# Kernel tuning notes

Hardware: AMD Instinct MI355X
Metric: run time of the kernel (lower is better)

The kernel has to match this reference:

```python
import jax, jax.numpy as jnp
import numpy as np

D_MODEL = 1024
N_HEADS = 16
HEAD_DIM = D_MODEL // N_HEADS


def setup_inputs() -> dict:
    key = jax.random.key(0)
    k1, k2, k3 = jax.random.split(key, 3)
    scale = 1.0 / np.sqrt(D_MODEL)
    x = jax.random.normal(k1, (4, 2048, D_MODEL), dtype=jnp.float32)
    w_qkv = jax.random.normal(k2, (D_MODEL, 3 * D_MODEL), dtype=jnp.float32) * scale
    b_qkv = jnp.zeros((3 * D_MODEL,), dtype=jnp.float32)
    w_proj = jax.random.normal(k3, (D_MODEL, D_MODEL), dtype=jnp.float32) * scale
    b_proj = jnp.zeros((D_MODEL,), dtype=jnp.float32)
    return {"x": x, "w_qkv": w_qkv, "b_qkv": b_qkv, "w_proj": w_proj, "b_proj": b_proj}


def reference(x, w_qkv, b_qkv, w_proj, b_proj):
    B, T, C = x.shape
    H, Dh = N_HEADS, HEAD_DIM
    qkv = x @ w_qkv + b_qkv                       # (B, T, 3C)
    qkv = qkv.reshape(B, T, 3, H, Dh)
    q = qkv[:, :, 0].transpose(0, 2, 1, 3)        # (B, H, T, Dh)
    k = qkv[:, :, 1].transpose(0, 2, 1, 3)
    v = qkv[:, :, 2].transpose(0, 2, 1, 3)
    att = jnp.einsum('bhqd,bhkd->bhqk', q, k) / jnp.sqrt(jnp.float32(Dh))
    causal = jnp.tril(jnp.ones((T, T), dtype=bool))
    att = jnp.where(causal[None, None], att, -jnp.inf)
    att = jax.nn.softmax(att, axis=-1)
    y = jnp.einsum('bhqk,bhkd->bhqd', att, v)     # (B, H, T, Dh)
    y = y.transpose(0, 2, 1, 3).reshape(B, T, C)
    return y @ w_proj + b_proj
```

## Files before the change

### kernel.cpp

```cpp
#include <hip/hip_runtime.h>
#include <hip/hip_bf16.h>
#include <math.h>

typedef __bf16 bf16_t;
typedef __bf16 bf16x4 __attribute__((ext_vector_type(4)));
typedef __bf16 bf16x8 __attribute__((ext_vector_type(8)));
typedef float floatx4 __attribute__((ext_vector_type(4)));

#define AS1 __attribute__((address_space(1)))
#define AS3 __attribute__((address_space(3)))

__device__ bf16_t g_xb[8192 * 1024];
__device__ bf16_t g_wqkvT[3072 * 1024];
__device__ bf16_t g_wprojT[1024 * 1024];
__device__ float  g_bqkv[3072];
__device__ float  g_bproj[1024];
__device__ bf16_t g_qkv[3ull * 64 * 2048 * 64];
#define HBREG (64ull * 2048 * 64)

__global__ __launch_bounds__(256) void cvt_x(const float* __restrict__ src, int n) {
  int i0 = (blockIdx.x * 256 + threadIdx.x) * 8;
  if (i0 >= n) return;
  const float4* s = (const float4*)src;
  float4 a = s[i0 / 4], b = s[i0 / 4 + 1];
  bf16x8 v;
  v[0] = (bf16_t)a.x; v[1] = (bf16_t)a.y; v[2] = (bf16_t)a.z; v[3] = (bf16_t)a.w;
  v[4] = (bf16_t)b.x; v[5] = (bf16_t)b.y; v[6] = (bf16_t)b.z; v[7] = (bf16_t)b.w;
  *(bf16x8*)&g_xb[i0] = v;
}

__global__ __launch_bounds__(256) void cvt_bias(const float* __restrict__ src,
                                                int which, int n) {
  int i = blockIdx.x * 256 + threadIdx.x;
  if (i >= n) return;
  (which ? g_bproj : g_bqkv)[i] = src[i];
}

__global__ __launch_bounds__(256) void tr64(const float* __restrict__ in,
                                            int which, int R, int C) {
  __shared__ bf16_t tile[64][65];
  bf16_t* out = which ? g_wprojT : g_wqkvT;
  int r0 = blockIdx.y * 64, c0 = blockIdx.x * 64;
  int tid = threadIdx.x;
#pragma unroll
  for (int it = 0; it < 16; ++it) {
    int idx = tid + it * 256;
    int r = idx >> 6, c = idx & 63;
    tile[r][c] = (bf16_t)in[(size_t)(r0 + r) * C + (c0 + c)];
  }
  __syncthreads();
#pragma unroll
  for (int it = 0; it < 16; ++it) {
    int idx = tid + it * 256;
    int r = idx >> 6, c = idx & 63;
    out[(size_t)(c0 + r) * R + (r0 + c)] = tile[c][r];
  }
}

__global__ __launch_bounds__(256) void gemm_bt(float* __restrict__ out_ext,
                                               int M, int N, int K,
                                               int amode, int bsel, int cmode) {
  __shared__ bf16_t As[128 * 32];
  __shared__ bf16_t Bs[128 * 32];
  const bf16_t* A = (amode == 0) ? g_xb : g_qkv;
  const bf16_t* Bt = bsel ? g_wprojT : g_wqkvT;
  const float* bias = bsel ? g_bproj : g_bqkv;
  const int tid = threadIdx.x;
  const int m0 = blockIdx.y * 128, n0 = blockIdx.x * 128;
  const int lane = tid & 63, wave = tid >> 6;
  const int wm = wave >> 1, wn = wave & 1;
  const int quad = lane >> 4, l16 = lane & 15;
  const int wub = tid & ~63;

  floatx4 acc[4][4] = {};

  for (int k0 = 0; k0 < K; k0 += 32) {
#pragma unroll
    for (int it = 0; it < 2; ++it) {
      int idx = tid + it * 256;
      int row = idx >> 2;
      int c8 = (idx & 3) * 8;
      int wbase = (it * 256 + wub) * 8;
      const bf16_t* asrc;
      if (amode == 0) {
        asrc = &A[(size_t)(m0 + row) * K + k0 + c8];
      } else {
        int m = m0 + row;
        int b = m >> 11, t = m & 2047;
        int h = k0 >> 6, dd = (k0 & 63) + c8;
        asrc = &A[((size_t)((b * 16 + h) * 2048 + t)) * 64 + dd];
      }
      const bf16_t* bsrc = &Bt[(size_t)(n0 + row) * K + k0 + c8];
      __builtin_amdgcn_global_load_lds((const AS1 void*)asrc,
                                       (AS3 void*)&As[wbase], 16, 0, 0);
      __builtin_amdgcn_global_load_lds((const AS1 void*)bsrc,
                                       (AS3 void*)&Bs[wbase], 16, 0, 0);
    }
    __syncthreads();
    bf16x8 af[4], bfr[4];
#pragma unroll
    for (int t = 0; t < 4; ++t) {
      af[t] = *(const bf16x8*)&As[(wm * 64 + t * 16 + l16) * 32 + quad * 8];
      bfr[t] = *(const bf16x8*)&Bs[(wn * 64 + t * 16 + l16) * 32 + quad * 8];
    }
#pragma unroll
    for (int tm = 0; tm < 4; ++tm)
#pragma unroll
      for (int tn = 0; tn < 4; ++tn)
        acc[tm][tn] = __builtin_amdgcn_mfma_f32_16x16x32_bf16(
            af[tm], bfr[tn], acc[tm][tn], 0, 0, 0);
    __syncthreads();
  }

#pragma unroll
  for (int tm = 0; tm < 4; ++tm) {
#pragma unroll
    for (int tn = 0; tn < 4; ++tn) {
      int ncol = n0 + wn * 64 + tn * 16 + l16;
      float bb = bias[ncol];
      int mbase = m0 + wm * 64 + tm * 16 + quad * 4;
      if (cmode == 0) {
        int which = ncol >> 10;
        int h = (ncol >> 6) & 15;
        int d = ncol & 63;
        int b = mbase >> 11, t = mbase & 2047;
        if (which == 2) {
          bf16x4 pk;
#pragma unroll
          for (int r = 0; r < 4; ++r) pk[r] = (bf16_t)(acc[tm][tn][r] + bb);
          size_t dst = 2 * HBREG + ((size_t)((b * 16 + h) * 64 + d)) * 2048 + t;
          *(bf16x4*)&g_qkv[dst] = pk;
        } else {
          size_t base = (size_t)which * HBREG +
                        ((size_t)((b * 16 + h) * 2048 + t)) * 64 + d;
#pragma unroll
          for (int r = 0; r < 4; ++r)
            g_qkv[base + (size_t)r * 64] = (bf16_t)(acc[tm][tn][r] + bb);
        }
      } else {
#pragma unroll
        for (int r = 0; r < 4; ++r)
          out_ext[(size_t)(mbase + r) * N + ncol] = acc[tm][tn][r] + bb;
      }
    }
  }
}

__global__ __launch_bounds__(256) void attn64() {
  const int LDW = 72;
  __shared__ bf16_t Qs[64 * 72];
  __shared__ bf16_t Ks[64 * 72];
  __shared__ bf16_t Vt[64 * 72];
  __shared__ bf16_t Ps[64 * 72];
  const float C1 = 0.1803368801111204f;
  const float C2 = -23.083120654223414f;
  const int tid = threadIdx.x;
  const int qpair = blockIdx.x;
  const int bh = blockIdx.y;
  const bf16_t* Qb  = g_qkv + (size_t)bh * 2048 * 64;
  const bf16_t* Kb  = g_qkv + HBREG + (size_t)bh * 2048 * 64;
  const bf16_t* VTb = g_qkv + 2 * HBREG + (size_t)bh * 64 * 2048;
  bf16_t* Yb = g_qkv + (size_t)bh * 2048 * 64;
  const int lane = tid & 63, wave = tid >> 6;
  const int quad = lane >> 4, l16 = lane & 15;
  const int row0 = tid >> 3, c80 = (tid & 7) * 8;

  bf16x8 ones8;
#pragma unroll
  for (int j = 0; j < 8; ++j) ones8[j] = (bf16_t)1.0f;

  for (int ph = 0; ph < 2; ++ph) {
    const int qi = ph ? (31 - qpair) : qpair;
    const int q0 = qi * 64;

    *(bf16x8*)&Qs[row0 * LDW + c80] =
        *(const bf16x8*)&Qb[(size_t)(q0 + row0) * 64 + c80];
    *(bf16x8*)&Qs[(row0 + 32) * LDW + c80] =
        *(const bf16x8*)&Qb[(size_t)(q0 + row0 + 32) * 64 + c80];
    __syncthreads();
    bf16x8 aq0 = *(const bf16x8*)&Qs[(wave * 16 + l16) * LDW + quad * 8];
    bf16x8 aq1 = *(const bf16x8*)&Qs[(wave * 16 + l16) * LDW + 32 + quad * 8];

    floatx4 o[4] = {};
    floatx4 osum = {};

    bf16x8 kp0 = *(const bf16x8*)&Kb[(size_t)row0 * 64 + c80];
    bf16x8 kp1 = *(const bf16x8*)&Kb[(size_t)(row0 + 32) * 64 + c80];
    bf16x8 vp0 = *(const bf16x8*)&VTb[(size_t)row0 * 2048 + c80];
    bf16x8 vp1 = *(const bf16x8*)&VTb[(size_t)(row0 + 32) * 2048 + c80];

    const int ntiles = qi + 1;
    for (int kt = 0; kt < ntiles; ++kt) {
      __syncthreads();
      *(bf16x8*)&Ks[row0 * LDW + c80] = kp0;
      *(bf16x8*)&Ks[(row0 + 32) * LDW + c80] = kp1;
      *(bf16x8*)&Vt[row0 * LDW + c80] = vp0;
      *(bf16x8*)&Vt[(row0 + 32) * LDW + c80] = vp1;
      if (kt + 1 < ntiles) {
        const int k1 = (kt + 1) * 64;
        kp0 = *(const bf16x8*)&Kb[(size_t)(k1 + row0) * 64 + c80];
        kp1 = *(const bf16x8*)&Kb[(size_t)(k1 + row0 + 32) * 64 + c80];
        vp0 = *(const bf16x8*)&VTb[(size_t)row0 * 2048 + k1 + c80];
        vp1 = *(const bf16x8*)&VTb[(size_t)(row0 + 32) * 2048 + k1 + c80];
      }
      __syncthreads();

      const int k0 = kt * 64;
      floatx4 s[4];
#pragma unroll
      for (int tn = 0; tn < 4; ++tn) {
        bf16x8 bk0 = *(const bf16x8*)&Ks[(tn * 16 + l16) * LDW + quad * 8];
        bf16x8 bk1 = *(const bf16x8*)&Ks[(tn * 16 + l16) * LDW + 32 + quad * 8];
        floatx4 z = {};
        z = __builtin_amdgcn_mfma_f32_16x16x32_bf16(aq0, bk0, z, 0, 0, 0);
        z = __builtin_amdgcn_mfma_f32_16x16x32_bf16(aq1, bk1, z, 0, 0, 0);
        s[tn] = z;
      }

      if (kt == qi) {
#pragma unroll
        for (int tn = 0; tn < 4; ++tn) {
          int kcol = k0 + tn * 16 + l16;
#pragma unroll
          for (int r = 0; r < 4; ++r) {
            int qrow = q0 + wave * 16 + quad * 4 + r;
            float p = exp2f(fminf(fmaf(s[tn][r], C1, C2), 30.f));
            s[tn][r] = (kcol > qrow) ? 0.f : p;
          }
        }
      } else {
#pragma unroll
        for (int tn = 0; tn < 4; ++tn)
#pragma unroll
          for (int r = 0; r < 4; ++r)
            s[tn][r] = exp2f(fminf(fmaf(s[tn][r], C1, C2), 30.f));
      }

      bf16_t* Pw = &Ps[wave * 16 * LDW];
#pragma unroll
      for (int tn = 0; tn < 4; ++tn)
#pragma unroll
        for (int r = 0; r < 4; ++r)
          Pw[(quad * 4 + r) * LDW + tn * 16 + l16] = (bf16_t)s[tn][r];

      bf16x8 ap0 = *(const bf16x8*)&Pw[l16 * LDW + quad * 8];
      bf16x8 ap1 = *(const bf16x8*)&Pw[l16 * LDW + 32 + quad * 8];
#pragma unroll
      for (int tn = 0; tn < 4; ++tn) {
        bf16x8 bv0 = *(const bf16x8*)&Vt[(tn * 16 + l16) * LDW + quad * 8];
        bf16x8 bv1 = *(const bf16x8*)&Vt[(tn * 16 + l16) * LDW + 32 + quad * 8];
        o[tn] = __builtin_amdgcn_mfma_f32_16x16x32_bf16(ap0, bv0, o[tn], 0, 0, 0);
        o[tn] = __builtin_amdgcn_mfma_f32_16x16x32_bf16(ap1, bv1, o[tn], 0, 0, 0);
      }
      osum = __builtin_amdgcn_mfma_f32_16x16x32_bf16(ap0, ones8, osum, 0, 0, 0);
      osum = __builtin_amdgcn_mfma_f32_16x16x32_bf16(ap1, ones8, osum, 0, 0, 0);
    }

#pragma unroll
    for (int tn = 0; tn < 4; ++tn) {
      int d = tn * 16 + l16;
#pragma unroll
      for (int r = 0; r < 4; ++r) {
        int t = q0 + wave * 16 + quad * 4 + r;
        float v = o[tn][r] / osum[r];
        Yb[(size_t)t * 64 + d] = (bf16_t)v;
      }
    }
    __syncthreads();
  }
}

extern "C" void kernel_launch(void* const* d_in, const int* in_sizes, int n_in,
                              void* d_out, int out_size, void* d_ws, size_t ws_size,
                              hipStream_t stream) {
  const float* x      = (const float*)d_in[0];
  const float* w_qkv  = (const float*)d_in[1];
  const float* b_qkv  = (const float*)d_in[2];
  const float* w_proj = (const float*)d_in[3];
  const float* b_proj = (const float*)d_in[4];
  (void)d_ws; (void)ws_size;

  cvt_x<<<4096, 256, 0, stream>>>(x, 8192 * 1024);
  cvt_bias<<<12, 256, 0, stream>>>(b_qkv, 0, 3072);
  cvt_bias<<<4, 256, 0, stream>>>(b_proj, 1, 1024);
  tr64<<<dim3(48, 16), 256, 0, stream>>>(w_qkv, 0, 1024, 3072);
  tr64<<<dim3(16, 16), 256, 0, stream>>>(w_proj, 1, 1024, 1024);

  gemm_bt<<<dim3(24, 64), 256, 0, stream>>>(nullptr, 8192, 3072, 1024, 0, 0, 0);

  attn64<<<dim3(16, 64), 256, 0, stream>>>();

  gemm_bt<<<dim3(8, 64), 256, 0, stream>>>((float*)d_out, 8192, 1024, 1024, 1, 1, 1);
}
```

Before: 321.2 us.

## Merge prep kernels, stage 64-wide K in GEMM, alias P onto Q in attention

Three changes. The bias-copy and x-conversion kernels are merged into one launch, and the two weight transposes into another, cutting the launch count from five to two. The GEMM now loads two 32-wide K slices per iteration into doubled shared buffers, which halves the number of barrier pairs per K step but is not true double-buffering, since loads and compute are still separated by a barrier. The attention kernel reuses the Q buffer for the P tile to save shared memory and possibly raise occupancy, which is only safe if Q is not needed after P is written.

Result: faster. 314.5 us (-2.1%).

```diff
diff --git a/kernel.cpp b/kernel.cpp
--- a/kernel.cpp
+++ b/kernel.cpp
@@ -18,29 +18,37 @@
 __device__ bf16_t g_qkv[3ull * 64 * 2048 * 64];
 #define HBREG (64ull * 2048 * 64)
 
-__global__ __launch_bounds__(256) void cvt_x(const float* __restrict__ src, int n) {
-  int i0 = (blockIdx.x * 256 + threadIdx.x) * 8;
-  if (i0 >= n) return;
-  const float4* s = (const float4*)src;
-  float4 a = s[i0 / 4], b = s[i0 / 4 + 1];
-  bf16x8 v;
-  v[0] = (bf16_t)a.x; v[1] = (bf16_t)a.y; v[2] = (bf16_t)a.z; v[3] = (bf16_t)a.w;
-  v[4] = (bf16_t)b.x; v[5] = (bf16_t)b.y; v[6] = (bf16_t)b.z; v[7] = (bf16_t)b.w;
-  *(bf16x8*)&g_xb[i0] = v;
-}
-
-__global__ __launch_bounds__(256) void cvt_bias(const float* __restrict__ src,
-                                                int which, int n) {
-  int i = blockIdx.x * 256 + threadIdx.x;
-  if (i >= n) return;
-  (which ? g_bproj : g_bqkv)[i] = src[i];
-}
-
-__global__ __launch_bounds__(256) void tr64(const float* __restrict__ in,
-                                            int which, int R, int C) {
+__global__ __launch_bounds__(256) void cvt_x(const float* __restrict__ src,
+                                             const float* __restrict__ bq,
+                                             const float* __restrict__ bp) {
+  int blk = blockIdx.x;
+  int tid = threadIdx.x;
+  if (blk < 4096) {
+    int i0 = (blk * 256 + tid) * 8;
+    const float4* s = (const float4*)src;
+    float4 a = s[i0 / 4], b = s[i0 / 4 + 1];
+    bf16x8 v;
+    v[0] = (bf16_t)a.x; v[1] = (bf16_t)a.y; v[2] = (bf16_t)a.z; v[3] = (bf16_t)a.w;
+    v[4] = (bf16_t)b.x; v[5] = (bf16_t)b.y; v[6] = (bf16_t)b.z; v[7] = (bf16_t)b.w;
+    *(bf16x8*)&g_xb[i0] = v;
+  } else if (blk == 4096) {
+    for (int i = tid; i < 3072; i += 256) g_bqkv[i] = bq[i];
+  } else {
+    for (int i = tid; i < 1024; i += 256) g_bproj[i] = bp[i];
+  }
+}
+
+__global__ __launch_bounds__(256) void tr64(const float* __restrict__ wqkv,
+                                            const float* __restrict__ wproj) {
   __shared__ bf16_t tile[64][65];
-  bf16_t* out = which ? g_wprojT : g_wqkvT;
-  int r0 = blockIdx.y * 64, c0 = blockIdx.x * 64;
+  const int R = 1024;
+  int bx = blockIdx.x;
+  const float* in;
+  bf16_t* out;
+  int C, c0;
+  if (bx < 48) { in = wqkv; out = g_wqkvT; C = 3072; c0 = bx * 64; }
+  else         { in = wproj; out = g_wprojT; C = 1024; c0 = (bx - 48) * 64; }
+  int r0 = blockIdx.y * 64;
   int tid = threadIdx.x;
 #pragma unroll
   for (int it = 0; it < 16; ++it) {
@@ -60,8 +68,8 @@
 __global__ __launch_bounds__(256) void gemm_bt(float* __restrict__ out_ext,
                                                int M, int N, int K,
                                                int amode, int bsel, int cmode) {
-  __shared__ bf16_t As[128 * 32];
-  __shared__ bf16_t Bs[128 * 32];
+  __shared__ bf16_t As[2][128 * 32];
+  __shared__ bf16_t Bs[2][128 * 32];
   const bf16_t* A = (amode == 0) ? g_xb : g_qkv;
   const bf16_t* Bt = bsel ? g_wprojT : g_wqkvT;
   const float* bias = bsel ? g_bproj : g_bqkv;
@@ -74,41 +82,48 @@
 
   floatx4 acc[4][4] = {};
 
-  for (int k0 = 0; k0 < K; k0 += 32) {
-#pragma unroll
-    for (int it = 0; it < 2; ++it) {
-      int idx = tid + it * 256;
-      int row = idx >> 2;
-      int c8 = (idx & 3) * 8;
-      int wbase = (it * 256 + wub) * 8;
-      const bf16_t* asrc;
-      if (amode == 0) {
-        asrc = &A[(size_t)(m0 + row) * K + k0 + c8];
-      } else {
-        int m = m0 + row;
-        int b = m >> 11, t = m & 2047;
-        int h = k0 >> 6, dd = (k0 & 63) + c8;
-        asrc = &A[((size_t)((b * 16 + h) * 2048 + t)) * 64 + dd];
-      }
-      const bf16_t* bsrc = &Bt[(size_t)(n0 + row) * K + k0 + c8];
-      __builtin_amdgcn_global_load_lds((const AS1 void*)asrc,
-                                       (AS3 void*)&As[wbase], 16, 0, 0);
-      __builtin_amdgcn_global_load_lds((const AS1 void*)bsrc,
-                                       (AS3 void*)&Bs[wbase], 16, 0, 0);
+  for (int k0 = 0; k0 < K; k0 += 64) {
+#pragma unroll
+    for (int sl = 0; sl < 2; ++sl) {
+      int kk0 = k0 + sl * 32;
+#pragma unroll
+      for (int it = 0; it < 2; ++it) {
+        int idx = tid + it * 256;
+        int row = idx >> 2;
+        int c8 = (idx & 3) * 8;
+        int wbase = (it * 256 + wub) * 8;
+        const bf16_t* asrc;
+        if (amode == 0) {
+          asrc = &A[(size_t)(m0 + row) * K + kk0 + c8];
+        } else {
+          int m = m0 + row;
+          int b = m >> 11, t = m & 2047;
+          int h = kk0 >> 6, dd = (kk0 & 63) + c8;
+          asrc = &A[((size_t)((b * 16 + h) * 2048 + t)) * 64 + dd];
+        }
+        const bf16_t* bsrc = &Bt[(size_t)(n0 + row) * K + kk0 + c8];
+        __builtin_amdgcn_global_load_lds((const AS1 void*)asrc,
+                                         (AS3 void*)&As[sl][wbase], 16, 0, 0);
+        __builtin_amdgcn_global_load_lds((const AS1 void*)bsrc,
+                                         (AS3 void*)&Bs[sl][wbase], 16, 0, 0);
+      }
     }
     __syncthreads();
-    bf16x8 af[4], bfr[4];
-#pragma unroll
-    for (int t = 0; t < 4; ++t) {
-      af[t] = *(const bf16x8*)&As[(wm * 64 + t * 16 + l16) * 32 + quad * 8];
-      bfr[t] = *(const bf16x8*)&Bs[(wn * 64 + t * 16 + l16) * 32 + quad * 8];
-    }
-#pragma unroll
-    for (int tm = 0; tm < 4; ++tm)
-#pragma unroll
-      for (int tn = 0; tn < 4; ++tn)
-        acc[tm][tn] = __builtin_amdgcn_mfma_f32_16x16x32_bf16(
-            af[tm], bfr[tn], acc[tm][tn], 0, 0, 0);
+#pragma unroll
+    for (int sl = 0; sl < 2; ++sl) {
+      bf16x8 af[4], bfr[4];
+#pragma unroll
+      for (int t = 0; t < 4; ++t) {
+        af[t] = *(const bf16x8*)&As[sl][(wm * 64 + t * 16 + l16) * 32 + quad * 8];
+        bfr[t] = *(const bf16x8*)&Bs[sl][(wn * 64 + t * 16 + l16) * 32 + quad * 8];
+      }
+#pragma unroll
+      for (int tm = 0; tm < 4; ++tm)
+#pragma unroll
+        for (int tn = 0; tn < 4; ++tn)
+          acc[tm][tn] = __builtin_amdgcn_mfma_f32_16x16x32_bf16(
+              af[tm], bfr[tn], acc[tm][tn], 0, 0, 0);
+    }
     __syncthreads();
   }
 
@@ -151,7 +166,7 @@
   __shared__ bf16_t Qs[64 * 72];
   __shared__ bf16_t Ks[64 * 72];
   __shared__ bf16_t Vt[64 * 72];
-  __shared__ bf16_t Ps[64 * 72];
+  bf16_t* Ps = Qs;
   const float C1 = 0.1803368801111204f;
   const float C2 = -23.083120654223414f;
   const int tid = threadIdx.x;
@@ -280,11 +295,8 @@
   const float* b_proj = (const float*)d_in[4];
   (void)d_ws; (void)ws_size;
 
-  cvt_x<<<4096, 256, 0, stream>>>(x, 8192 * 1024);
-  cvt_bias<<<12, 256, 0, stream>>>(b_qkv, 0, 3072);
-  cvt_bias<<<4, 256, 0, stream>>>(b_proj, 1, 1024);
-  tr64<<<dim3(48, 16), 256, 0, stream>>>(w_qkv, 0, 1024, 3072);
-  tr64<<<dim3(16, 16), 256, 0, stream>>>(w_proj, 1, 1024, 1024);
+  cvt_x<<<4098, 256, 0, stream>>>(x, b_qkv, b_proj);
+  tr64<<<dim3(64, 16), 256, 0, stream>>>(w_qkv, w_proj);
 
   gemm_bt<<<dim3(24, 64), 256, 0, stream>>>(nullptr, 8192, 3072, 1024, 0, 0, 0);
 
```
